# Performance work log

Hardware: AMD Instinct MI355X
Metric: run time of the kernel (lower is better)

The kernel has to match this reference:

```python
import jax, jax.numpy as jnp
import numpy as np

EMBED_DIM = 768
NUM_HEADS = 12
HEAD_DIM = EMBED_DIM // NUM_HEADS
SCALE = HEAD_DIM ** -0.5


def setup_inputs() -> dict:
    key = jax.random.key(0)
    k1, k2, k3, k4, k5 = jax.random.split(key, 5)
    B, T = 8, 1024
    hidden_states = jax.random.normal(k1, (B, T, EMBED_DIM), dtype=jnp.float32)
    init = 0.02
    qkv_w = jax.random.normal(k2, (EMBED_DIM, 3 * EMBED_DIM), dtype=jnp.float32) * init
    qkv_b = jnp.zeros((3 * EMBED_DIM,), dtype=jnp.float32)
    proj_w = jax.random.normal(k3, (EMBED_DIM, EMBED_DIM), dtype=jnp.float32) * init
    proj_b = jnp.zeros((EMBED_DIM,), dtype=jnp.float32)
    return {
        "hidden_states": hidden_states,
        "qkv_w": qkv_w,
        "qkv_b": qkv_b,
        "proj_w": proj_w,
        "proj_b": proj_b,
    }


def reference(hidden_states, qkv_w, qkv_b, proj_w, proj_b):
    B, T, C = hidden_states.shape
    # fused QKV projection
    mixed = hidden_states @ qkv_w + qkv_b            # [B, T, 3C]
    mixed = mixed.reshape(B, T, 3, NUM_HEADS, HEAD_DIM)
    mixed = jnp.transpose(mixed, (2, 0, 3, 1, 4))    # [3, B, H, T, D]
    q, k, v = mixed[0], mixed[1], mixed[2]
    # scaled dot-product attention (dropout is identity in eval)
    scores = jnp.einsum("bhqd,bhkd->bhqk", q, k) * SCALE
    probs = jax.nn.softmax(scores, axis=-1)
    ctx = jnp.einsum("bhqk,bhkd->bhqd", probs, v)    # [B, H, T, D]
    ctx = jnp.transpose(ctx, (0, 2, 1, 3)).reshape(B, T, C)
    out = ctx @ proj_w + proj_b
    return out
```

## Files before the change

### kernel.cpp

```cpp
#include <hip/hip_runtime.h>

#define EMBED 768
#define NHEAD 12
#define HDIM 64
#define BATCH 8
#define SEQ 1024
#define ROWS (BATCH*SEQ)
#define QKVN (3*EMBED)
#define ATTN_SCALE 0.125f

typedef short s16x8 __attribute__((ext_vector_type(8)));
typedef float f32x4 __attribute__((ext_vector_type(4)));

__device__ __forceinline__ float bf2f(unsigned short u) {
    union { unsigned int i; float f; } v; v.i = ((unsigned int)u) << 16; return v.f;
}
__device__ __forceinline__ unsigned short f2bf(float f) {
    unsigned int i = __builtin_bit_cast(unsigned int, f);
    i += 0x7FFFu + ((i >> 16) & 1u);
    return (unsigned short)(i >> 16);
}

__device__ __forceinline__ void async16(short* lds, const unsigned short* g) {
    __builtin_amdgcn_global_load_lds(
        (const __attribute__((address_space(1))) unsigned int*)g,
        (__attribute__((address_space(3))) unsigned int*)lds,
        16, 0, 0);
}

__global__ __launch_bounds__(256) void prep_k(
    const float* __restrict__ qkv_w, unsigned short* __restrict__ WqkvT,
    const float* __restrict__ proj_w, unsigned short* __restrict__ WprojT,
    const float* __restrict__ hidden, unsigned short* __restrict__ hiddenBf)
{
    int blk = blockIdx.x;
    if (blk < 6912) {
        int tid = blk * 256 + threadIdx.x;
        int n = tid / EMBED, k = tid - n * EMBED;
        WqkvT[tid] = f2bf(qkv_w[k * QKVN + n]);
    } else if (blk < 9216) {
        int tid = (blk - 6912) * 256 + threadIdx.x;
        int n = tid / EMBED, k = tid - n * EMBED;
        WprojT[tid] = f2bf(proj_w[k * EMBED + n]);
    } else {
        int tid = (blk - 9216) * 256 + threadIdx.x;
        int base = tid * 8;
        float4 f0 = *(const float4*)&hidden[base];
        float4 f1 = *(const float4*)&hidden[base + 4];
        s16x8 a;
        a[0] = (short)f2bf(f0.x); a[1] = (short)f2bf(f0.y);
        a[2] = (short)f2bf(f0.z); a[3] = (short)f2bf(f0.w);
        a[4] = (short)f2bf(f1.x); a[5] = (short)f2bf(f1.y);
        a[6] = (short)f2bf(f1.z); a[7] = (short)f2bf(f1.w);
        *(s16x8*)&hiddenBf[base] = a;
    }
}

template <int OUT_F32>
__global__ __launch_bounds__(256) void gemm128(
    const unsigned short* __restrict__ A,
    const unsigned short* __restrict__ Bt,
    const float* __restrict__ bias,
    void* __restrict__ Cv,
    int M, int N, int K)
{
    __shared__ short As[128 * 32];
    __shared__ short Bs[128 * 32];
    int t = threadIdx.x, lane = t & 63, w = t >> 6;
    int quad = lane >> 4, low = lane & 15;
    int m0 = blockIdx.x * 128, n0 = blockIdx.y * 128;
    int wm = (w & 1) * 64, wn = (w >> 1) * 64;

    int ci0 = w * 128 + lane;
    int r0 = ci0 >> 2, c0 = (ci0 & 3) ^ ((r0 >> 1) & 3);
    int ci1 = ci0 + 64;
    int r1 = ci1 >> 2, c1 = (ci1 & 3) ^ ((r1 >> 1) & 3);
    const unsigned short* pa0 = A + (long long)(m0 + r0) * K + c0 * 8;
    const unsigned short* pa1 = A + (long long)(m0 + r1) * K + c1 * 8;
    const unsigned short* pb0 = Bt + (long long)(n0 + r0) * K + c0 * 8;
    const unsigned short* pb1 = Bt + (long long)(n0 + r1) * K + c1 * 8;
    short* la0 = As + (w * 128) * 8;
    short* la1 = As + (w * 128 + 64) * 8;
    short* lb0 = Bs + (w * 128) * 8;
    short* lb1 = Bs + (w * 128 + 64) * 8;

    f32x4 acc[4][4] = {};
    for (int k0 = 0; k0 < K; k0 += 32) {
        __syncthreads();
        async16(la0, pa0 + k0);
        async16(la1, pa1 + k0);
        async16(lb0, pb0 + k0);
        async16(lb1, pb1 + k0);
        __syncthreads();
        s16x8 af[4], bfr[4];
        #pragma unroll
        for (int i = 0; i < 4; i++) {
            int ra = wm + i * 16 + low;
            af[i] = *(const s16x8*)&As[ra * 32 + ((quad ^ ((ra >> 1) & 3)) * 8)];
            int rb = wn + i * 16 + low;
            bfr[i] = *(const s16x8*)&Bs[rb * 32 + ((quad ^ ((rb >> 1) & 3)) * 8)];
        }
        #pragma unroll
        for (int i = 0; i < 4; i++)
            #pragma unroll
            for (int j = 0; j < 4; j++)
                acc[i][j] = __builtin_amdgcn_mfma_f32_16x16x32_bf16(af[i], bfr[j], acc[i][j], 0, 0, 0);
    }
    #pragma unroll
    for (int i = 0; i < 4; i++)
        #pragma unroll
        for (int j = 0; j < 4; j++)
            #pragma unroll
            for (int r = 0; r < 4; r++) {
                int m = m0 + wm + i * 16 + quad * 4 + r;
                int n = n0 + wn + j * 16 + low;
                float v = acc[i][j][r] + bias[n];
                if (OUT_F32) ((float*)Cv)[(long long)m * N + n] = v;
                else ((unsigned short*)Cv)[(long long)m * N + n] = f2bf(v);
            }
}

__global__ __launch_bounds__(256) void attn_k(
    const unsigned short* __restrict__ mixed,
    unsigned short* __restrict__ ctx)
{
    __shared__ short Ks[64 * 72];
    __shared__ short Vt[64 * 72];
    __shared__ short Pl[4 * 16 * 72];
    int blk = blockIdx.x;
    int qc = blk & 15;
    int bh = blk >> 4;
    int b = bh / NHEAD, h = bh - b * NHEAD;
    int t = threadIdx.x;
    int lane = t & 63, w = t >> 6;
    int quad = lane >> 4, low = lane & 15;
    long long rowbase = (long long)b * SEQ;
    int q0 = qc * 64 + w * 16;
    int hoff = h * HDIM;

    s16x8 qf[2];
    {
        long long r = (rowbase + q0 + low) * QKVN + hoff;
        qf[0] = *(const s16x8*)&mixed[r + quad * 8];
        qf[1] = *(const s16x8*)&mixed[r + 32 + quad * 8];
    }

    f32x4 o[4] = {};
    float lsum[4] = {0.f, 0.f, 0.f, 0.f};

    int skv = t >> 2;
    int sd = (t & 3) * 16;

    for (int kv0 = 0; kv0 < SEQ; kv0 += 64) {
        __syncthreads();
        long long krow = (rowbase + kv0 + skv) * QKVN + EMBED + hoff + sd;
        *(s16x8*)&Ks[skv * 72 + sd]     = *(const s16x8*)&mixed[krow];
        *(s16x8*)&Ks[skv * 72 + sd + 8] = *(const s16x8*)&mixed[krow + 8];
        long long vrow = (rowbase + kv0 + skv) * QKVN + 2 * EMBED + hoff + sd;
        s16x8 v0 = *(const s16x8*)&mixed[vrow];
        s16x8 v1 = *(const s16x8*)&mixed[vrow + 8];
        #pragma unroll
        for (int i = 0; i < 8; i++) {
            int d = sd + i;
            Vt[d * 72 + (skv ^ (((d >> 3) & 7) << 3))] = v0[i];
        }
        #pragma unroll
        for (int i = 0; i < 8; i++) {
            int d = sd + 8 + i;
            Vt[d * 72 + (skv ^ (((d >> 3) & 7) << 3))] = v1[i];
        }
        __syncthreads();

        f32x4 s[4] = {};
        #pragma unroll
        for (int n = 0; n < 4; n++) {
            s16x8 b0 = *(const s16x8*)&Ks[(n * 16 + low) * 72 + quad * 8];
            s16x8 b1 = *(const s16x8*)&Ks[(n * 16 + low) * 72 + 32 + quad * 8];
            s[n] = __builtin_amdgcn_mfma_f32_16x16x32_bf16(qf[0], b0, s[n], 0, 0, 0);
            s[n] = __builtin_amdgcn_mfma_f32_16x16x32_bf16(qf[1], b1, s[n], 0, 0, 0);
        }

        short* pw = &Pl[w * 16 * 72];
        #pragma unroll
        for (int n = 0; n < 4; n++)
            #pragma unroll
            for (int r = 0; r < 4; r++) {
                float e = __expf(s[n][r] * ATTN_SCALE);
                lsum[r] += e;
                pw[(quad * 4 + r) * 72 + n * 16 + low] = (short)f2bf(e);
            }

        s16x8 pf0 = *(const s16x8*)&pw[low * 72 + quad * 8];
        s16x8 pf1 = *(const s16x8*)&pw[low * 72 + 32 + quad * 8];

        #pragma unroll
        for (int nt = 0; nt < 4; nt++) {
            int d = nt * 16 + low;
            int key = (d >> 3) & 7;
            s16x8 vf0 = *(const s16x8*)&Vt[d * 72 + ((quad ^ key) << 3)];
            s16x8 vf1 = *(const s16x8*)&Vt[d * 72 + (((4 + quad) ^ key) << 3)];
            o[nt] = __builtin_amdgcn_mfma_f32_16x16x32_bf16(pf0, vf0, o[nt], 0, 0, 0);
            o[nt] = __builtin_amdgcn_mfma_f32_16x16x32_bf16(pf1, vf1, o[nt], 0, 0, 0);
        }
    }

    #pragma unroll
    for (int off = 1; off < 16; off <<= 1)
        #pragma unroll
        for (int r = 0; r < 4; r++)
            lsum[r] += __shfl_xor(lsum[r], off, 64);

    #pragma unroll
    for (int nt = 0; nt < 4; nt++)
        #pragma unroll
        for (int r = 0; r < 4; r++) {
            int q = q0 + quad * 4 + r;
            ctx[(rowbase + q) * EMBED + hoff + nt * 16 + low] = f2bf(o[nt][r] / lsum[r]);
        }
}

extern "C" void kernel_launch(void* const* d_in, const int* in_sizes, int n_in,
                              void* d_out, int out_size, void* d_ws, size_t ws_size,
                              hipStream_t stream) {
    const float* hidden = (const float*)d_in[0];
    const float* qkv_w  = (const float*)d_in[1];
    const float* qkv_b  = (const float*)d_in[2];
    const float* proj_w = (const float*)d_in[3];
    const float* proj_b = (const float*)d_in[4];
    float* out = (float*)d_out;

    char* ws = (char*)d_ws;
    unsigned short* hiddenBf = (unsigned short*)ws;
    unsigned short* ctx      = (unsigned short*)ws;
    unsigned short* WqkvT    = (unsigned short*)(ws + 12582912);
    unsigned short* WprojT   = (unsigned short*)(ws + 16121856);
    unsigned short* mixed    = (unsigned short*)(ws + 17301504);

    prep_k<<<dim3(12288), 256, 0, stream>>>(qkv_w, WqkvT, proj_w, WprojT, hidden, hiddenBf);
    gemm128<0><<<dim3(ROWS / 128, QKVN / 128), 256, 0, stream>>>(
        hiddenBf, WqkvT, qkv_b, mixed, ROWS, QKVN, EMBED);
    attn_k<<<dim3(96 * 16), 256, 0, stream>>>(mixed, ctx);
    gemm128<1><<<dim3(ROWS / 128, EMBED / 128), 256, 0, stream>>>(
        ctx, WprojT, proj_b, out, ROWS, EMBED, EMBED);
}
```

Before: 225.8 us.

## Tile weight transpose through LDS and double query rows per attention warp

The weight transpose in the prep kernel now goes through a padded 64x65 shared-memory tile, so both the fp32 reads and the bf16 writes are coalesced instead of strided gathers. The attention kernel gives each wave 32 query rows instead of 16, so each K/V tile loaded into LDS is reused twice as much and half as many blocks reload K/V. In exchange the attention kernel uses more registers and launches only 768 blocks, which may lower occupancy or leave the GPU underfilled.

```diff
diff --git a/kernel.cpp b/kernel.cpp
--- a/kernel.cpp
+++ b/kernel.cpp
@@ -33,17 +33,28 @@
     const float* __restrict__ proj_w, unsigned short* __restrict__ WprojT,
     const float* __restrict__ hidden, unsigned short* __restrict__ hiddenBf)
 {
+    __shared__ float tile[64][65];
     int blk = blockIdx.x;
-    if (blk < 6912) {
-        int tid = blk * 256 + threadIdx.x;
-        int n = tid / EMBED, k = tid - n * EMBED;
-        WqkvT[tid] = f2bf(qkv_w[k * QKVN + n]);
-    } else if (blk < 9216) {
-        int tid = (blk - 6912) * 256 + threadIdx.x;
-        int n = tid / EMBED, k = tid - n * EMBED;
-        WprojT[tid] = f2bf(proj_w[k * EMBED + n]);
+    int t = threadIdx.x;
+    if (blk < 576) {
+        const float* in; unsigned short* outp; int K, N, tx, ty;
+        if (blk < 432) { in = qkv_w; outp = WqkvT; K = EMBED; N = QKVN; tx = blk % 36; ty = blk / 36; }
+        else { int b2 = blk - 432; in = proj_w; outp = WprojT; K = EMBED; N = EMBED; tx = b2 % 12; ty = b2 / 12; }
+        int n0 = tx * 64, k0 = ty * 64;
+        int c = t & 63, r0 = t >> 6;
+        #pragma unroll
+        for (int i = 0; i < 16; i++) {
+            int r = r0 * 16 + i;
+            tile[r][c] = in[(long long)(k0 + r) * N + n0 + c];
+        }
+        __syncthreads();
+        #pragma unroll
+        for (int i = 0; i < 16; i++) {
+            int nr = r0 * 16 + i;
+            outp[(long long)(n0 + nr) * K + k0 + c] = f2bf(tile[c][nr]);
+        }
     } else {
-        int tid = (blk - 9216) * 256 + threadIdx.x;
+        int tid = (blk - 576) * 256 + t;
         int base = tid * 8;
         float4 f0 = *(const float4*)&hidden[base];
         float4 f1 = *(const float4*)&hidden[base + 4];
@@ -126,27 +137,28 @@
 {
     __shared__ short Ks[64 * 72];
     __shared__ short Vt[64 * 72];
-    __shared__ short Pl[4 * 16 * 72];
+    __shared__ short Pl[4 * 32 * 72];
     int blk = blockIdx.x;
-    int qc = blk & 15;
-    int bh = blk >> 4;
+    int qc = blk & 7;
+    int bh = blk >> 3;
     int b = bh / NHEAD, h = bh - b * NHEAD;
     int t = threadIdx.x;
     int lane = t & 63, w = t >> 6;
     int quad = lane >> 4, low = lane & 15;
     long long rowbase = (long long)b * SEQ;
-    int q0 = qc * 64 + w * 16;
+    int q0 = qc * 128 + w * 32;
     int hoff = h * HDIM;
 
-    s16x8 qf[2];
-    {
-        long long r = (rowbase + q0 + low) * QKVN + hoff;
-        qf[0] = *(const s16x8*)&mixed[r + quad * 8];
-        qf[1] = *(const s16x8*)&mixed[r + 32 + quad * 8];
-    }
-
-    f32x4 o[4] = {};
-    float lsum[4] = {0.f, 0.f, 0.f, 0.f};
+    s16x8 qf[2][2];
+    #pragma unroll
+    for (int qh = 0; qh < 2; qh++) {
+        long long r = (rowbase + q0 + qh * 16 + low) * QKVN + hoff;
+        qf[qh][0] = *(const s16x8*)&mixed[r + quad * 8];
+        qf[qh][1] = *(const s16x8*)&mixed[r + 32 + quad * 8];
+    }
+
+    f32x4 o[2][4] = {};
+    float lsum[2][4] = {};
 
     int skv = t >> 2;
     int sd = (t & 3) * 16;
@@ -171,27 +183,35 @@
         }
         __syncthreads();
 
-        f32x4 s[4] = {};
+        f32x4 s[2][4] = {};
         #pragma unroll
         for (int n = 0; n < 4; n++) {
             s16x8 b0 = *(const s16x8*)&Ks[(n * 16 + low) * 72 + quad * 8];
             s16x8 b1 = *(const s16x8*)&Ks[(n * 16 + low) * 72 + 32 + quad * 8];
-            s[n] = __builtin_amdgcn_mfma_f32_16x16x32_bf16(qf[0], b0, s[n], 0, 0, 0);
-            s[n] = __builtin_amdgcn_mfma_f32_16x16x32_bf16(qf[1], b1, s[n], 0, 0, 0);
-        }
-
-        short* pw = &Pl[w * 16 * 72];
-        #pragma unroll
-        for (int n = 0; n < 4; n++)
-            #pragma unroll
-            for (int r = 0; r < 4; r++) {
-                float e = __expf(s[n][r] * ATTN_SCALE);
-                lsum[r] += e;
-                pw[(quad * 4 + r) * 72 + n * 16 + low] = (short)f2bf(e);
-            }
-
-        s16x8 pf0 = *(const s16x8*)&pw[low * 72 + quad * 8];
-        s16x8 pf1 = *(const s16x8*)&pw[low * 72 + 32 + quad * 8];
+            s[0][n] = __builtin_amdgcn_mfma_f32_16x16x32_bf16(qf[0][0], b0, s[0][n], 0, 0, 0);
+            s[0][n] = __builtin_amdgcn_mfma_f32_16x16x32_bf16(qf[0][1], b1, s[0][n], 0, 0, 0);
+            s[1][n] = __builtin_amdgcn_mfma_f32_16x16x32_bf16(qf[1][0], b0, s[1][n], 0, 0, 0);
+            s[1][n] = __builtin_amdgcn_mfma_f32_16x16x32_bf16(qf[1][1], b1, s[1][n], 0, 0, 0);
+        }
+
+        short* pw = &Pl[w * 32 * 72];
+        #pragma unroll
+        for (int qh = 0; qh < 2; qh++)
+            #pragma unroll
+            for (int n = 0; n < 4; n++)
+                #pragma unroll
+                for (int r = 0; r < 4; r++) {
+                    float e = __expf(s[qh][n][r] * ATTN_SCALE);
+                    lsum[qh][r] += e;
+                    pw[(qh * 16 + quad * 4 + r) * 72 + n * 16 + low] = (short)f2bf(e);
+                }
+
+        s16x8 pf[2][2];
+        #pragma unroll
+        for (int qh = 0; qh < 2; qh++) {
+            pf[qh][0] = *(const s16x8*)&pw[(qh * 16 + low) * 72 + quad * 8];
+            pf[qh][1] = *(const s16x8*)&pw[(qh * 16 + low) * 72 + 32 + quad * 8];
+        }
 
         #pragma unroll
         for (int nt = 0; nt < 4; nt++) {
@@ -199,24 +219,31 @@
             int key = (d >> 3) & 7;
             s16x8 vf0 = *(const s16x8*)&Vt[d * 72 + ((quad ^ key) << 3)];
             s16x8 vf1 = *(const s16x8*)&Vt[d * 72 + (((4 + quad) ^ key) << 3)];
-            o[nt] = __builtin_amdgcn_mfma_f32_16x16x32_bf16(pf0, vf0, o[nt], 0, 0, 0);
-            o[nt] = __builtin_amdgcn_mfma_f32_16x16x32_bf16(pf1, vf1, o[nt], 0, 0, 0);
+            o[0][nt] = __builtin_amdgcn_mfma_f32_16x16x32_bf16(pf[0][0], vf0, o[0][nt], 0, 0, 0);
+            o[0][nt] = __builtin_amdgcn_mfma_f32_16x16x32_bf16(pf[0][1], vf1, o[0][nt], 0, 0, 0);
+            o[1][nt] = __builtin_amdgcn_mfma_f32_16x16x32_bf16(pf[1][0], vf0, o[1][nt], 0, 0, 0);
+            o[1][nt] = __builtin_amdgcn_mfma_f32_16x16x32_bf16(pf[1][1], vf1, o[1][nt], 0, 0, 0);
         }
     }
 
     #pragma unroll
     for (int off = 1; off < 16; off <<= 1)
         #pragma unroll
-        for (int r = 0; r < 4; r++)
-            lsum[r] += __shfl_xor(lsum[r], off, 64);
-
-    #pragma unroll
-    for (int nt = 0; nt < 4; nt++)
-        #pragma unroll
-        for (int r = 0; r < 4; r++) {
-            int q = q0 + quad * 4 + r;
-            ctx[(rowbase + q) * EMBED + hoff + nt * 16 + low] = f2bf(o[nt][r] / lsum[r]);
-        }
+        for (int qh = 0; qh < 2; qh++)
+            #pragma unroll
+            for (int r = 0; r < 4; r++)
+                lsum[qh][r] += __shfl_xor(lsum[qh][r], off, 64);
+
+    #pragma unroll
+    for (int qh = 0; qh < 2; qh++)
+        #pragma unroll
+        for (int nt = 0; nt < 4; nt++)
+            #pragma unroll
+            for (int r = 0; r < 4; r++) {
+                int q = q0 + qh * 16 + quad * 4 + r;
+                ctx[(rowbase + q) * EMBED + hoff + nt * 16 + low] =
+                    f2bf(o[qh][nt][r] / lsum[qh][r]);
+            }
 }
 
 extern "C" void kernel_launch(void* const* d_in, const int* in_sizes, int n_in,
@@ -236,10 +263,10 @@
     unsigned short* WprojT   = (unsigned short*)(ws + 16121856);
     unsigned short* mixed    = (unsigned short*)(ws + 17301504);
 
-    prep_k<<<dim3(12288), 256, 0, stream>>>(qkv_w, WqkvT, proj_w, WprojT, hidden, hiddenBf);
+    prep_k<<<dim3(3648), 256, 0, stream>>>(qkv_w, WqkvT, proj_w, WprojT, hidden, hiddenBf);
     gemm128<0><<<dim3(ROWS / 128, QKVN / 128), 256, 0, stream>>>(
         hiddenBf, WqkvT, qkv_b, mixed, ROWS, QKVN, EMBED);
-    attn_k<<<dim3(96 * 16), 256, 0, stream>>>(mixed, ctx);
+    attn_k<<<dim3(96 * 8), 256, 0, stream>>>(mixed, ctx);
     gemm128<1><<<dim3(ROWS / 128, EMBED / 128), 256, 0, stream>>>(
         ctx, WprojT, proj_b, out, ROWS, EMBED, EMBED);
 }
```

Measured after the change: 208.2 us. 1.08x faster.
